# Performance work log

Hardware: AMD Instinct MI355X
Metric: run time of the kernel (lower is better)

The kernel has to match this reference:

```python
import jax, jax.numpy as jnp
import numpy as np

DIM = 1024
N_HEADS = 16
HEAD_DIM = DIM // N_HEADS
D_LATENT = 256
B, T = 1, 4096


def setup_inputs() -> dict:
    key = jax.random.key(0)
    ks = jax.random.split(key, 6)
    s = 0.02
    return {
        "x": jax.random.normal(ks[0], (B, T, DIM), dtype=jnp.float32),
        "W_DKV": jax.random.normal(ks[1], (DIM, D_LATENT), dtype=jnp.float32) * s,
        "W_UK": jax.random.normal(ks[2], (D_LATENT, DIM), dtype=jnp.float32) * s,
        "W_UV": jax.random.normal(ks[3], (D_LATENT, DIM), dtype=jnp.float32) * s,
        "W_UQ": jax.random.normal(ks[4], (DIM, DIM), dtype=jnp.float32) * s,
        "W_O": jax.random.normal(ks[5], (DIM, DIM), dtype=jnp.float32) * s,
    }


def reference(x, W_DKV, W_UK, W_UV, W_UQ, W_O):
    b, t, d = x.shape
    h, hd = N_HEADS, HEAD_DIM
    # low-rank latent KV projection
    c_kv = x @ W_DKV                                   # (b, t, d_latent)
    k = (c_kv @ W_UK).reshape(b, t, h, hd)             # (b, t, h, hd)
    v = (c_kv @ W_UV).reshape(b, t, h, hd)
    q = (x @ W_UQ).reshape(b, t, h, hd)
    scale = 1.0 / jnp.sqrt(jnp.asarray(hd, x.dtype))
    scores = jnp.einsum("bqhd,bkhd->bhqk", q, k) * scale   # (b, h, t, t)
    causal = jnp.tril(jnp.ones((t, t), dtype=bool))
    scores = jnp.where(causal, scores, jnp.asarray(-jnp.inf, scores.dtype))
    probs = jax.nn.softmax(scores, axis=-1)            # dropout is eval-mode identity
    ctx = jnp.einsum("bhqk,bkhd->bqhd", probs, v).reshape(b, t, d)
    return ctx @ W_O
```

## Files before the change

kernel.cpp:

```cpp
#include <hip/hip_runtime.h>
#include <hip/hip_bf16.h>
#include <stdint.h>

#define T_SEQ 4096
#define DIMX 1024
#define NH 16
#define HD 64
#define DLAT 256

typedef __bf16 bf16x8 __attribute__((ext_vector_type(8)));
typedef __bf16 bf16x4 __attribute__((ext_vector_type(4)));
typedef float floatx4 __attribute__((ext_vector_type(4)));

#define MFMA(a, b, c) __builtin_amdgcn_mfma_f32_16x16x32_bf16(a, b, c, 0, 0, 0)

__device__ inline void gload_lds16(const __bf16* g, __bf16* l) {
  __builtin_amdgcn_global_load_lds(
      (const __attribute__((address_space(1))) uint32_t*)g,
      (__attribute__((address_space(3))) uint32_t*)l, 16, 0, 0);
}

__global__ __launch_bounds__(256) void prep_kernel(
    const float* __restrict__ x, const float* __restrict__ wdkv,
    const float* __restrict__ wuk, const float* __restrict__ wuv,
    const float* __restrict__ wuq, const float* __restrict__ wo,
    __bf16* __restrict__ x_bf, __bf16* __restrict__ wt_dkv,
    __bf16* __restrict__ wt_uk, __bf16* __restrict__ wt_uv,
    __bf16* __restrict__ wt_uq, __bf16* __restrict__ wt_o) {
  int id = blockIdx.x;
  if (id < 2048) {
    int i = id * 256 + threadIdx.x;
    const float4* p = (const float4*)x;
    float4 a = p[2 * i], b = p[2 * i + 1];
    bf16x8 r = {(__bf16)a.x, (__bf16)a.y, (__bf16)a.z, (__bf16)a.w,
                (__bf16)b.x, (__bf16)b.y, (__bf16)b.z, (__bf16)b.w};
    *(bf16x8*)(x_bf + 8 * (size_t)i) = r;
    return;
  }
  int t = id - 2048;
  const float* in;
  __bf16* out;
  int R, C, lt;
  if (t < 64)       { in = wdkv; out = wt_dkv; R = 1024; C = 256;  lt = t; }
  else if (t < 128) { in = wuk;  out = wt_uk;  R = 256;  C = 1024; lt = t - 64; }
  else if (t < 192) { in = wuv;  out = wt_uv;  R = 256;  C = 1024; lt = t - 128; }
  else if (t < 448) { in = wuq;  out = wt_uq;  R = 1024; C = 1024; lt = t - 192; }
  else              { in = wo;   out = wt_o;   R = 1024; C = 1024; lt = t - 448; }
  __shared__ __bf16 tls[64][65];
  int tpr = C >> 6;
  int r0 = (lt / tpr) * 64, c0 = (lt % tpr) * 64;
  int tid = threadIdx.x;
#pragma unroll
  for (int i = 0; i < 16; i++) {
    int idx = tid + i * 256;
    int r = idx >> 6, c = idx & 63;
    tls[r][c] = (__bf16)in[(size_t)(r0 + r) * C + c0 + c];
  }
  __syncthreads();
#pragma unroll
  for (int i = 0; i < 16; i++) {
    int idx = tid + i * 256;
    int rr = idx & 63, cc = idx >> 6;
    out[(size_t)(c0 + cc) * R + r0 + rr] = tls[rr][cc];
  }
}

#define BUFE 4096
#define BUFEB 2048

__global__ __launch_bounds__(256) void gemm_a64(const __bf16* __restrict__ A,
                                                const __bf16* __restrict__ B1,
                                                const __bf16* __restrict__ B2,
                                                __bf16* __restrict__ C1,
                                                __bf16* __restrict__ C2) {
  __shared__ __attribute__((aligned(16))) __bf16 Al[2][BUFE];
  __shared__ __attribute__((aligned(16))) __bf16 Bl[2][BUFEB];
  int tid = threadIdx.x;
  int w = tid >> 6, lane = tid & 63;
  int quad = lane >> 4, l16 = lane & 15;
  int mw = w & 1, nw = w >> 1;
  int bx = blockIdx.x, m0 = blockIdx.y * 128;
  const __bf16* Bt;
  __bf16* C;
  int n0, N;
  float sc;
  if (bx < 4) { Bt = B1; C = C1; n0 = bx * 64; N = DLAT; sc = 1.0f; }
  else        { Bt = B2; C = C2; n0 = (bx - 4) * 64; N = DIMX;
                sc = 0.125f * 1.44269504088896340736f; }
  const int K = DIMX;
  int arow = w * 32 + (lane >> 2), acol = (lane & 3) << 3;
  int brow = w * 16 + (lane >> 2);

  floatx4 acc[4][2];
#pragma unroll
  for (int i = 0; i < 4; i++)
#pragma unroll
    for (int j = 0; j < 2; j++) acc[i][j] = (floatx4){0.f, 0.f, 0.f, 0.f};

  for (int k0 = 0; k0 < K; k0 += 64) {
#pragma unroll
    for (int kh = 0; kh < 2; kh++) {
#pragma unroll
      for (int j = 0; j < 2; j++)
        gload_lds16(A + (size_t)(m0 + arow + j * 16) * K + k0 + kh * 32 + acol,
                    &Al[kh][(w * 32 + j * 16) * 32]);
      gload_lds16(Bt + (size_t)(n0 + brow) * K + k0 + kh * 32 + acol,
                  &Bl[kh][(w * 16) * 32]);
    }
    __syncthreads();
#pragma unroll
    for (int kh = 0; kh < 2; kh++) {
      bf16x8 af[4], bfr[2];
#pragma unroll
      for (int mt = 0; mt < 4; mt++)
        af[mt] =
            *(const bf16x8*)&Al[kh][(mw * 64 + mt * 16 + l16) * 32 + quad * 8];
#pragma unroll
      for (int nt = 0; nt < 2; nt++)
        bfr[nt] =
            *(const bf16x8*)&Bl[kh][(nw * 32 + nt * 16 + l16) * 32 + quad * 8];
#pragma unroll
      for (int mt = 0; mt < 4; mt++)
#pragma unroll
        for (int nt = 0; nt < 2; nt++)
          acc[mt][nt] = MFMA(af[mt], bfr[nt], acc[mt][nt]);
    }
    __syncthreads();
  }
#pragma unroll
  for (int mt = 0; mt < 4; mt++)
#pragma unroll
    for (int nt = 0; nt < 2; nt++)
#pragma unroll
      for (int r = 0; r < 4; r++) {
        int row = m0 + mw * 64 + mt * 16 + quad * 4 + r;
        int col = n0 + nw * 32 + nt * 16 + l16;
        C[(size_t)row * N + col] = (__bf16)(acc[mt][nt][r] * sc);
      }
}

__global__ __launch_bounds__(256) void gemm_kv128(const __bf16* __restrict__ A,
                                                  const __bf16* __restrict__ Bk,
                                                  const __bf16* __restrict__ Bv,
                                                  __bf16* __restrict__ k,
                                                  __bf16* __restrict__ vt) {
  __shared__ __attribute__((aligned(16))) __bf16 Al[2][BUFE];
  __shared__ __attribute__((aligned(16))) __bf16 Bl[2][BUFE];
  __shared__ __attribute__((aligned(16))) __bf16 tw[4][64 * 72];
  int tid = threadIdx.x;
  int w = tid >> 6, lane = tid & 63;
  int quad = lane >> 4, l16 = lane & 15;
  int mw = w & 1, nw = w >> 1;
  int bx = blockIdx.x, m0 = blockIdx.y * 128;
  bool is_k = (bx < 8);
  const __bf16* Bt = is_k ? Bk : Bv;
  int n0 = (is_k ? bx : bx - 8) * 128;
  const int K = DLAT;
  int arow = w * 32 + (lane >> 2), acol = (lane & 3) << 3;

  floatx4 acc[4][4];
#pragma unroll
  for (int i = 0; i < 4; i++)
#pragma unroll
    for (int j = 0; j < 4; j++) acc[i][j] = (floatx4){0.f, 0.f, 0.f, 0.f};

  for (int k0 = 0; k0 < K; k0 += 64) {
#pragma unroll
    for (int kh = 0; kh < 2; kh++)
#pragma unroll
      for (int j = 0; j < 2; j++) {
        gload_lds16(A + (size_t)(m0 + arow + j * 16) * K + k0 + kh * 32 + acol,
                    &Al[kh][(w * 32 + j * 16) * 32]);
        gload_lds16(Bt + (size_t)(n0 + arow + j * 16) * K + k0 + kh * 32 + acol,
                    &Bl[kh][(w * 32 + j * 16) * 32]);
      }
    __syncthreads();
#pragma unroll
    for (int kh = 0; kh < 2; kh++) {
      bf16x8 af[4], bfr[4];
#pragma unroll
      for (int mt = 0; mt < 4; mt++)
        af[mt] =
            *(const bf16x8*)&Al[kh][(mw * 64 + mt * 16 + l16) * 32 + quad * 8];
#pragma unroll
      for (int nt = 0; nt < 4; nt++)
        bfr[nt] =
            *(const bf16x8*)&Bl[kh][(nw * 64 + nt * 16 + l16) * 32 + quad * 8];
#pragma unroll
      for (int mt = 0; mt < 4; mt++)
#pragma unroll
        for (int nt = 0; nt < 4; nt++)
          acc[mt][nt] = MFMA(af[mt], bfr[nt], acc[mt][nt]);
    }
    __syncthreads();
  }
  if (is_k) {
#pragma unroll
    for (int mt = 0; mt < 4; mt++)
#pragma unroll
      for (int nt = 0; nt < 4; nt++)
#pragma unroll
        for (int r = 0; r < 4; r++) {
          int row = m0 + mw * 64 + mt * 16 + quad * 4 + r;
          int col = n0 + nw * 64 + nt * 16 + l16;
          k[(size_t)row * DIMX + col] = (__bf16)acc[mt][nt][r];
        }
  } else {
#pragma unroll
    for (int mt = 0; mt < 4; mt++)
#pragma unroll
      for (int nt = 0; nt < 4; nt++)
#pragma unroll
        for (int r = 0; r < 4; r++)
          tw[w][(nt * 16 + l16) * 72 + mt * 16 + quad * 4 + r] =
              (__bf16)acc[mt][nt][r];
    int cbase = lane >> 3, chunk = lane & 7;
#pragma unroll
    for (int i = 0; i < 8; i++) {
      int c = cbase + i * 8;
      bf16x8 v8 = *(const bf16x8*)&tw[w][c * 72 + chunk * 8];
      *(bf16x8*)&vt[(size_t)(n0 + nw * 64 + c) * T_SEQ + m0 + mw * 64 +
                    chunk * 8] = v8;
    }
  }
}

__global__ __launch_bounds__(256) void gemm_f64(const __bf16* __restrict__ A,
                                                const __bf16* __restrict__ Bt,
                                                float* __restrict__ C) {
  __shared__ __attribute__((aligned(16))) __bf16 Al[2][BUFE];
  __shared__ __attribute__((aligned(16))) __bf16 Bl[2][BUFEB];
  int tid = threadIdx.x;
  int w = tid >> 6, lane = tid & 63;
  int quad = lane >> 4, l16 = lane & 15;
  int mw = w & 1, nw = w >> 1;
  int n0 = blockIdx.x * 64, m0 = blockIdx.y * 128;
  const int K = DIMX, N = DIMX;
  int arow = w * 32 + (lane >> 2), acol = (lane & 3) << 3;
  int brow = w * 16 + (lane >> 2);

  floatx4 acc[4][2];
#pragma unroll
  for (int i = 0; i < 4; i++)
#pragma unroll
    for (int j = 0; j < 2; j++) acc[i][j] = (floatx4){0.f, 0.f, 0.f, 0.f};

  for (int k0 = 0; k0 < K; k0 += 64) {
#pragma unroll
    for (int kh = 0; kh < 2; kh++) {
#pragma unroll
      for (int j = 0; j < 2; j++)
        gload_lds16(A + (size_t)(m0 + arow + j * 16) * K + k0 + kh * 32 + acol,
                    &Al[kh][(w * 32 + j * 16) * 32]);
      gload_lds16(Bt + (size_t)(n0 + brow) * K + k0 + kh * 32 + acol,
                  &Bl[kh][(w * 16) * 32]);
    }
    __syncthreads();
#pragma unroll
    for (int kh = 0; kh < 2; kh++) {
      bf16x8 af[4], bfr[2];
#pragma unroll
      for (int mt = 0; mt < 4; mt++)
        af[mt] =
            *(const bf16x8*)&Al[kh][(mw * 64 + mt * 16 + l16) * 32 + quad * 8];
#pragma unroll
      for (int nt = 0; nt < 2; nt++)
        bfr[nt] =
            *(const bf16x8*)&Bl[kh][(nw * 32 + nt * 16 + l16) * 32 + quad * 8];
#pragma unroll
      for (int mt = 0; mt < 4; mt++)
#pragma unroll
        for (int nt = 0; nt < 2; nt++)
          acc[mt][nt] = MFMA(af[mt], bfr[nt], acc[mt][nt]);
    }
    __syncthreads();
  }
#pragma unroll
  for (int mt = 0; mt < 4; mt++)
#pragma unroll
    for (int nt = 0; nt < 2; nt++)
#pragma unroll
      for (int r = 0; r < 4; r++) {
        int row = m0 + mw * 64 + mt * 16 + quad * 4 + r;
        int col = n0 + nw * 32 + nt * 16 + l16;
        C[(size_t)row * N + col] = acc[mt][nt][r];
      }
}

#define PST 72
__global__ __launch_bounds__(256, 3) void mla_attn11(
    const __bf16* __restrict__ Q, const __bf16* __restrict__ Kg,
    const __bf16* __restrict__ Vt, __bf16* __restrict__ ctx) {
  __shared__ __attribute__((aligned(16))) __bf16 Kl[2][64 * 64];
  __shared__ __attribute__((aligned(16))) __bf16 Vl[2][64 * 64];
  __shared__ __attribute__((aligned(16))) __bf16 Pl[64 * PST];
  int tid = threadIdx.x;
  int wave = tid >> 6, lane = tid & 63;
  int quad = lane >> 4, l16 = lane & 15;
  int h = blockIdx.x;
  int qt = 63 - blockIdx.y;
  int q0 = qt * 64;
  int srow = tid >> 3, pos = tid & 7;
  int gco = pos << 3;
  int sw = (pos ^ (srow & 7)) << 3;
  int swr = srow * 64 + sw;
  int fr = (wave * 16 + l16) * PST;
  int c0s = ((quad ^ (l16 & 7)) << 3);
  int c1s = (((4 + quad) ^ (l16 & 7)) << 3);

  *(bf16x8*)&Pl[srow * PST + gco] =
      *(const bf16x8*)&Q[(size_t)(q0 + srow) * DIMX + h * HD + gco];
  *(bf16x8*)&Pl[(srow + 32) * PST + gco] =
      *(const bf16x8*)&Q[(size_t)(q0 + srow + 32) * DIMX + h * HD + gco];
  *(bf16x8*)&Kl[0][swr] =
      *(const bf16x8*)&Kg[(size_t)srow * DIMX + h * HD + gco];
  *(bf16x8*)&Kl[0][swr + 2048] =
      *(const bf16x8*)&Kg[(size_t)(srow + 32) * DIMX + h * HD + gco];
  *(bf16x8*)&Vl[0][swr] =
      *(const bf16x8*)&Vt[(size_t)(h * HD + srow) * T_SEQ + gco];
  *(bf16x8*)&Vl[0][swr + 2048] =
      *(const bf16x8*)&Vt[(size_t)(h * HD + srow + 32) * T_SEQ + gco];
  __syncthreads();
  bf16x8 qf0 = *(const bf16x8*)&Pl[fr + quad * 8];
  bf16x8 qf1 = *(const bf16x8*)&Pl[fr + 32 + quad * 8];

  floatx4 o[4];
  float lsum = 0.f;
#pragma unroll
  for (int i = 0; i < 4; i++) o[i] = (floatx4){0.f, 0.f, 0.f, 0.f};

  for (int kt = 0; kt <= qt; kt++) {
    int cur = kt & 1, nxt = cur ^ 1;
    bool pre = (kt < qt);
    bf16x8 kp0, kp1, vp0, vp1;
    if (pre) {
      int k0n = (kt + 1) * 64;
      kp0 = *(const bf16x8*)&Kg[(size_t)(k0n + srow) * DIMX + h * HD + gco];
      kp1 = *(const bf16x8*)&Kg[(size_t)(k0n + srow + 32) * DIMX + h * HD + gco];
      vp0 = *(const bf16x8*)&Vt[(size_t)(h * HD + srow) * T_SEQ + k0n + gco];
      vp1 = *(const bf16x8*)&Vt[(size_t)(h * HD + srow + 32) * T_SEQ + k0n + gco];
    }
    const __bf16* Kc = Kl[cur];
    const __bf16* Vc = Vl[cur];
    floatx4 s[4];
    __builtin_amdgcn_s_setprio(1);
#pragma unroll
    for (int ct = 0; ct < 4; ct++) {
      int rb = (ct * 16 + l16) * 64;
      bf16x8 kf0 = *(const bf16x8*)&Kc[rb + c0s];
      bf16x8 kf1 = *(const bf16x8*)&Kc[rb + c1s];
      floatx4 z = (floatx4){0.f, 0.f, 0.f, 0.f};
      z = MFMA(kf0, qf0, z);
      z = MFMA(kf1, qf1, z);
      s[ct] = z;
    }
    __builtin_amdgcn_s_setprio(0);
    bool diag = (kt == qt);
#pragma unroll
    for (int ct = 0; ct < 4; ct++) {
      float p0[4];
#pragma unroll
      for (int r = 0; r < 4; r++) {
        float p = __builtin_amdgcn_exp2f(s[ct][r]);
        if (diag && (ct * 16 + quad * 4 + r > wave * 16 + l16)) p = 0.f;
        lsum += p;
        p0[r] = p;
      }
      bf16x4 pk = {(__bf16)p0[0], (__bf16)p0[1], (__bf16)p0[2], (__bf16)p0[3]};
      *(bf16x4*)&Pl[(wave * 16 + l16) * PST + ct * 16 + quad * 4] = pk;
    }
    bf16x8 pf0 = *(const bf16x8*)&Pl[fr + quad * 8];
    bf16x8 pf1 = *(const bf16x8*)&Pl[fr + 32 + quad * 8];
    __builtin_amdgcn_s_setprio(1);
#pragma unroll
    for (int dt = 0; dt < 4; dt++) {
      int rb = (dt * 16 + l16) * 64;
      bf16x8 vf0 = *(const bf16x8*)&Vc[rb + c0s];
      bf16x8 vf1 = *(const bf16x8*)&Vc[rb + c1s];
      o[dt] = MFMA(pf0, vf0, o[dt]);
      o[dt] = MFMA(pf1, vf1, o[dt]);
    }
    __builtin_amdgcn_s_setprio(0);
    if (pre) {
      *(bf16x8*)&Kl[nxt][swr] = kp0;
      *(bf16x8*)&Kl[nxt][swr + 2048] = kp1;
      *(bf16x8*)&Vl[nxt][swr] = vp0;
      *(bf16x8*)&Vl[nxt][swr + 2048] = vp1;
    }
    __syncthreads();
  }

  lsum += __shfl_xor(lsum, 16, 64);
  lsum += __shfl_xor(lsum, 32, 64);
  float inv[4];
#pragma unroll
  for (int r = 0; r < 4; r++) inv[r] = 1.0f / __shfl(lsum, quad * 4 + r, 16);

#pragma unroll
  for (int dt = 0; dt < 4; dt++)
#pragma unroll
    for (int r = 0; r < 4; r++) {
      float val = o[dt][r] * inv[r];
      int row = q0 + wave * 16 + quad * 4 + r;
      int col = h * HD + dt * 16 + l16;
      ctx[(size_t)row * DIMX + col] = (__bf16)val;
    }
}

extern "C" void kernel_launch(void* const* d_in, const int* in_sizes, int n_in,
                              void* d_out, int out_size, void* d_ws,
                              size_t ws_size, hipStream_t stream) {
  const float* x = (const float*)d_in[0];
  const float* wdkv = (const float*)d_in[1];
  const float* wuk = (const float*)d_in[2];
  const float* wuv = (const float*)d_in[3];
  const float* wuq = (const float*)d_in[4];
  const float* wo = (const float*)d_in[5];
  float* out = (float*)d_out;

  __bf16* ws = (__bf16*)d_ws;
  __bf16* x_bf = ws;
  __bf16* q = x_bf + (size_t)T_SEQ * DIMX;
  __bf16* k = q + (size_t)T_SEQ * DIMX;
  __bf16* vt = k + (size_t)T_SEQ * DIMX;
  __bf16* ctx = vt + (size_t)T_SEQ * DIMX;
  __bf16* ckv = ctx + (size_t)T_SEQ * DIMX;
  __bf16* wt_dkv = ckv + (size_t)T_SEQ * DLAT;
  __bf16* wt_uk = wt_dkv + (size_t)DLAT * DIMX;
  __bf16* wt_uv = wt_uk + (size_t)DIMX * DLAT;
  __bf16* wt_uq = wt_uv + (size_t)DIMX * DLAT;
  __bf16* wt_o = wt_uq + (size_t)DIMX * DIMX;

  dim3 blk(256);
  prep_kernel<<<dim3(2752), blk, 0, stream>>>(x, wdkv, wuk, wuv, wuq, wo, x_bf,
                                              wt_dkv, wt_uk, wt_uv, wt_uq, wt_o);
  gemm_a64<<<dim3(20, T_SEQ / 128), blk, 0, stream>>>(x_bf, wt_dkv, wt_uq,
                                                      ckv, q);
  gemm_kv128<<<dim3(16, T_SEQ / 128), blk, 0, stream>>>(ckv, wt_uk, wt_uv, k,
                                                        vt);
  mla_attn11<<<dim3(NH, 64), dim3(256), 0, stream>>>(q, k, vt, ctx);
  gemm_f64<<<dim3(DIMX / 64, T_SEQ / 128), blk, 0, stream>>>(ctx, wt_o, out);
}
```

Before: 189.4 us.

## Stream K/V tiles into LDS via direct global-to-LDS loads and vectorize transpose stores

The attention kernel now prefetches the next K and V tiles with global_load_lds, writing straight into the swizzled LDS buffer. This removes the register staging and the separate LDS store pass, and lowers register pressure. The XOR swizzle moves to the global address side, so each lane fetches a permuted chunk that lands at a linear LDS position. Separately, the weight-transpose prep kernel now writes 8 bf16 values per store instead of one. The direct loads have no explicit wait before the barrier, which may depend on the compiler inserting vmcnt waits.

```diff
diff --git a/kernel.cpp b/kernel.cpp
--- a/kernel.cpp
+++ b/kernel.cpp
@@ -58,10 +58,14 @@
   }
   __syncthreads();
 #pragma unroll
-  for (int i = 0; i < 16; i++) {
+  for (int i = 0; i < 2; i++) {
     int idx = tid + i * 256;
-    int rr = idx & 63, cc = idx >> 6;
-    out[(size_t)(c0 + cc) * R + r0 + rr] = tls[rr][cc];
+    int cc = idx >> 3;
+    int rr8 = (idx & 7) * 8;
+    bf16x8 v;
+#pragma unroll
+    for (int j = 0; j < 8; j++) v[j] = tls[rr8 + j][cc];
+    *(bf16x8*)&out[(size_t)(c0 + cc) * R + r0 + rr8] = v;
   }
 }
 
@@ -288,7 +292,7 @@
 }
 
 #define PST 72
-__global__ __launch_bounds__(256, 3) void mla_attn11(
+__global__ __launch_bounds__(256, 3) void mla_attn12(
     const __bf16* __restrict__ Q, const __bf16* __restrict__ Kg,
     const __bf16* __restrict__ Vt, __bf16* __restrict__ ctx) {
   __shared__ __attribute__((aligned(16))) __bf16 Kl[2][64 * 64];
@@ -303,23 +307,19 @@
   int srow = tid >> 3, pos = tid & 7;
   int gco = pos << 3;
   int sw = (pos ^ (srow & 7)) << 3;
-  int swr = srow * 64 + sw;
   int fr = (wave * 16 + l16) * PST;
   int c0s = ((quad ^ (l16 & 7)) << 3);
   int c1s = (((4 + quad) ^ (l16 & 7)) << 3);
+  int wb = wave * 512;
 
   *(bf16x8*)&Pl[srow * PST + gco] =
       *(const bf16x8*)&Q[(size_t)(q0 + srow) * DIMX + h * HD + gco];
   *(bf16x8*)&Pl[(srow + 32) * PST + gco] =
       *(const bf16x8*)&Q[(size_t)(q0 + srow + 32) * DIMX + h * HD + gco];
-  *(bf16x8*)&Kl[0][swr] =
-      *(const bf16x8*)&Kg[(size_t)srow * DIMX + h * HD + gco];
-  *(bf16x8*)&Kl[0][swr + 2048] =
-      *(const bf16x8*)&Kg[(size_t)(srow + 32) * DIMX + h * HD + gco];
-  *(bf16x8*)&Vl[0][swr] =
-      *(const bf16x8*)&Vt[(size_t)(h * HD + srow) * T_SEQ + gco];
-  *(bf16x8*)&Vl[0][swr + 2048] =
-      *(const bf16x8*)&Vt[(size_t)(h * HD + srow + 32) * T_SEQ + gco];
+  gload_lds16(&Kg[(size_t)srow * DIMX + h * HD + sw], &Kl[0][wb]);
+  gload_lds16(&Kg[(size_t)(srow + 32) * DIMX + h * HD + sw], &Kl[0][2048 + wb]);
+  gload_lds16(&Vt[(size_t)(h * HD + srow) * T_SEQ + sw], &Vl[0][wb]);
+  gload_lds16(&Vt[(size_t)(h * HD + srow + 32) * T_SEQ + sw], &Vl[0][2048 + wb]);
   __syncthreads();
   bf16x8 qf0 = *(const bf16x8*)&Pl[fr + quad * 8];
   bf16x8 qf1 = *(const bf16x8*)&Pl[fr + 32 + quad * 8];
@@ -332,13 +332,16 @@
   for (int kt = 0; kt <= qt; kt++) {
     int cur = kt & 1, nxt = cur ^ 1;
     bool pre = (kt < qt);
-    bf16x8 kp0, kp1, vp0, vp1;
     if (pre) {
       int k0n = (kt + 1) * 64;
-      kp0 = *(const bf16x8*)&Kg[(size_t)(k0n + srow) * DIMX + h * HD + gco];
-      kp1 = *(const bf16x8*)&Kg[(size_t)(k0n + srow + 32) * DIMX + h * HD + gco];
-      vp0 = *(const bf16x8*)&Vt[(size_t)(h * HD + srow) * T_SEQ + k0n + gco];
-      vp1 = *(const bf16x8*)&Vt[(size_t)(h * HD + srow + 32) * T_SEQ + k0n + gco];
+      gload_lds16(&Kg[(size_t)(k0n + srow) * DIMX + h * HD + sw],
+                  &Kl[nxt][wb]);
+      gload_lds16(&Kg[(size_t)(k0n + srow + 32) * DIMX + h * HD + sw],
+                  &Kl[nxt][2048 + wb]);
+      gload_lds16(&Vt[(size_t)(h * HD + srow) * T_SEQ + k0n + sw],
+                  &Vl[nxt][wb]);
+      gload_lds16(&Vt[(size_t)(h * HD + srow + 32) * T_SEQ + k0n + sw],
+                  &Vl[nxt][2048 + wb]);
     }
     const __bf16* Kc = Kl[cur];
     const __bf16* Vc = Vl[cur];
@@ -381,12 +384,6 @@
       o[dt] = MFMA(pf1, vf1, o[dt]);
     }
     __builtin_amdgcn_s_setprio(0);
-    if (pre) {
-      *(bf16x8*)&Kl[nxt][swr] = kp0;
-      *(bf16x8*)&Kl[nxt][swr + 2048] = kp1;
-      *(bf16x8*)&Vl[nxt][swr] = vp0;
-      *(bf16x8*)&Vl[nxt][swr + 2048] = vp1;
-    }
     __syncthreads();
   }
 
@@ -438,6 +435,6 @@
                                                       ckv, q);
   gemm_kv128<<<dim3(16, T_SEQ / 128), blk, 0, stream>>>(ckv, wt_uk, wt_uv, k,
                                                         vt);
-  mla_attn11<<<dim3(NH, 64), dim3(256), 0, stream>>>(q, k, vt, ctx);
+  mla_attn12<<<dim3(NH, 64), dim3(256), 0, stream>>>(q, k, vt, ctx);
   gemm_f64<<<dim3(DIMX / 64, T_SEQ / 128), blk, 0, stream>>>(ctx, wt_o, out);
 }
```

Result: no change. 189.9 us (median of 2 runs) (+0.2%).
